# Kernel tuning notes

Measured on AMD Instinct MI355X. Metric: run time of the kernel, lower is better.

## Reference

```python
import jax, jax.numpy as jnp
import numpy as np

EPS = 1e-5


def _bn(x, g, b):
    # training-mode BatchNorm2d over (N, H, W), biased variance
    m = jnp.mean(x, axis=(0, 2, 3), keepdims=True)
    v = jnp.var(x, axis=(0, 2, 3), keepdims=True)
    return (x - m) * jax.lax.rsqrt(v + EPS) * g[None, :, None, None] + b[None, :, None, None]


def _conv1x1(x, w):
    # x: [B, Cin, H, W], w: [Cout, Cin]
    return jnp.einsum('bchw,oc->bohw', x, w)


def _prop_attention(x, wq, wkv, wo, bo, obj_dict, bg_dict, rand_inds):
    B, C, H, W = x.shape  # B == 1
    heads, crop = rand_inds.shape[0], rand_inds.shape[1]
    dh = C // heads
    HW = H * W
    num_obj = crop // 2
    # original does x.clone().detach() before attention
    xd = jax.lax.stop_gradient(x)
    xh = xd.reshape(heads, dh, HW)  # batch=1 folded away (matches t.view(-1, crop**2))
    # pos[h, i, j] = flat pixel index gathered for head h, group i, slot j
    pos = jnp.concatenate(
        [obj_dict[rand_inds[:, :num_obj]], bg_dict[rand_inds[:, num_obj:]]], axis=1
    )  # [heads, crop, crop]
    tokens = jax.vmap(lambda xv, pv: xv[:, pv])(xh, pos)  # [heads, dh, crop, crop]
    tokens = tokens.transpose(0, 2, 3, 1).reshape(heads * crop, crop, dh)
    q = tokens @ wq.T
    k, v = jnp.split(tokens @ wkv.T, 2, axis=-1)
    dots = jnp.einsum('bie,bje->bij', q, k) * (dh ** -0.5)
    attn = jax.nn.softmax(dots, axis=-1)
    out = jnp.einsum('bij,bje->bie', attn, v)  # [heads*crop, crop, dh]
    # faithful to torch out.view(heads*crop, -1, crop): a raw row-major reinterpret
    out_r = out.reshape(heads, crop, dh, crop)
    vals = out_r.transpose(0, 2, 1, 3).reshape(heads, dh, crop * crop)
    pos_flat = pos.reshape(heads, crop * crop)
    # pos is a bijection onto [0, HW) per head -> invert and gather
    ar = jnp.arange(HW, dtype=jnp.int32)
    inv = jax.vmap(lambda p: jnp.zeros((HW,), jnp.int32).at[p].set(ar))(pos_flat)
    img = jax.vmap(lambda vh, ih: vh[:, ih])(vals, inv)  # [heads, dh, HW]
    img = img.reshape(1, heads * dh, H, W)
    # to_out: Linear(dim, dim) applied channels-last
    return jnp.einsum('bchw,oc->bohw', img, wo) + bo[None, :, None, None]


def setup_inputs():
    H = W = 300
    HW = H * W
    heads, crop = 2, H
    num_obj = crop // 2
    ch, emb = 256, 64
    dh = emb // heads
    key = jax.random.key(0)
    ks = jax.random.split(key, 10)
    x = jax.random.normal(ks[0], (1, ch, H, W), jnp.float32)
    perm = jax.random.permutation(ks[1], HW)
    obj_dict = perm[: HW // 2]
    bg_dict = perm[HW // 2 :]
    ri = []
    for h in range(heads):
        po = jax.random.permutation(jax.random.fold_in(ks[2], h), HW // 2).reshape(num_obj, crop)
        pb = jax.random.permutation(jax.random.fold_in(ks[3], h), HW // 2).reshape(crop - num_obj, crop)
        ri.append(jnp.concatenate([po, pb], axis=0))
    rand_inds = jnp.stack(ri)  # [heads, crop, crop]
    w_conv1 = jax.random.normal(ks[4], (emb, ch), jnp.float32) / np.sqrt(ch)
    wq = jax.random.normal(ks[5], (dh, dh), jnp.float32) / np.sqrt(dh)
    wkv = jax.random.normal(ks[6], (2 * dh, dh), jnp.float32) / np.sqrt(dh)
    wo = jax.random.normal(ks[7], (emb, emb), jnp.float32) / np.sqrt(emb)
    bo = jnp.zeros((emb,), jnp.float32)
    w_conv2 = jax.random.normal(ks[8], (emb, 2 * emb), jnp.float32) / np.sqrt(2 * emb)
    return {
        'x': x,
        'w_conv1': w_conv1,
        'bn1_g': jnp.ones((emb,), jnp.float32),
        'bn1_b': jnp.zeros((emb,), jnp.float32),
        'wq': wq,
        'wkv': wkv,
        'wo': wo,
        'bo': bo,
        'w_conv2': w_conv2,
        'bn2_g': jnp.ones((emb,), jnp.float32),
        'bn2_b': jnp.zeros((emb,), jnp.float32),
        'obj_dict': obj_dict,
        'bg_dict': bg_dict,
        'rand_inds': rand_inds,
    }


def reference(x, w_conv1, bn1_g, bn1_b, wq, wkv, wo, bo, w_conv2, bn2_g, bn2_b, obj_dict, bg_dict, rand_inds):
    x1 = jax.nn.relu(_bn(_conv1x1(x, w_conv1), bn1_g, bn1_b))
    xa = jax.nn.relu(_prop_attention(x1, wq, wkv, wo, bo, obj_dict, bg_dict, rand_inds))
    xc = jnp.concatenate([xa, x1], axis=1)
    return jax.nn.relu(_bn(_conv1x1(xc, w_conv2), bn2_g, bn2_b))
```

## Files before the change

kernel.cpp:

```cpp
#include <hip/hip_runtime.h>
#include <hip/hip_bf16.h>

#define HW 90000
#define CROP 300
#define C2EXP 0.25503492f

typedef __attribute__((ext_vector_type(8))) short s8v;
typedef __attribute__((ext_vector_type(4))) float f4v;
#define MFMA16(a,b,c) __builtin_amdgcn_mfma_f32_16x16x32_bf16(a,b,c,0,0,0)

__device__ __forceinline__ unsigned short f2bf(float f) {
    unsigned int u = __float_as_uint(f);
    return (unsigned short)((u + 0x7fffu + ((u >> 16) & 1u)) >> 16);
}
__device__ __forceinline__ float bf2f(unsigned short s) {
    return __uint_as_float(((unsigned int)s) << 16);
}
__device__ __forceinline__ unsigned pk_trunc(float a, float b) {
    return __builtin_amdgcn_perm(__float_as_uint(b), __float_as_uint(a), 0x07060302u);
}
__device__ __forceinline__ unsigned pk_rne(float a, float b) {
    return (unsigned)f2bf(a) | ((unsigned)f2bf(b) << 16);
}

__global__ void prep_kernel(const float* __restrict__ w1, const float* __restrict__ wq,
                            const float* __restrict__ wkv, const float* __restrict__ wo,
                            const float* __restrict__ w2,
                            short* __restrict__ w1b, short* __restrict__ wkvb,
                            short* __restrict__ wob, short* __restrict__ w2b,
                            short* __restrict__ msb) {
    int idx = blockIdx.x * blockDim.x + threadIdx.x;
    int stride = gridDim.x * blockDim.x;
    for (int i = idx; i < 16384; i += stride) w1b[i] = (short)f2bf(w1[i]);
    for (int i = idx; i < 2048; i += stride)  wkvb[i] = (short)f2bf(wkv[i]);
    for (int i = idx; i < 4096; i += stride)  wob[i] = (short)f2bf(wo[i]);
    for (int i = idx; i < 8192; i += stride)  w2b[i] = (short)f2bf(w2[i]);
    for (int i = idx; i < 1024; i += stride) {
        int ep = i >> 5, e = i & 31;
        float s = 0.f;
        for (int a = 0; a < 32; ++a) s += wq[a * 32 + e] * wkv[a * 32 + ep];
        msb[i] = (short)f2bf(s * C2EXP);
    }
}

__global__ __launch_bounds__(256, 4) void conv1_mfma(const float* __restrict__ x,
        const short* __restrict__ w1b, short* __restrict__ y1b, float* __restrict__ stat) {
    __shared__ __align__(16) short lw[16384];
    __shared__ float red[2][4][64];
    const int wave = threadIdx.x >> 6, lane = threadIdx.x & 63;
    const int q = lane >> 4, n = lane & 15;
    for (int i = threadIdx.x; i < 2048; i += 256)
        ((uint4*)lw)[i] = ((const uint4*)w1b)[i];
    __syncthreads();

    const int s0 = blockIdx.x * 128 + wave * 32;
    int pbx = s0 + 2 * n;
    if (pbx > HW - 2) pbx = HW - 2;
    f4v acc[2][4];
#pragma unroll
    for (int mt = 0; mt < 2; ++mt)
#pragma unroll
        for (int nt = 0; nt < 4; ++nt) acc[mt][nt] = f4v{0.f, 0.f, 0.f, 0.f};

    float2 cur[8], nxt[8];
#pragma unroll
    for (int j = 0; j < 8; ++j)
        cur[j] = *(const float2*)(x + (size_t)(q * 8 + j) * HW + pbx);
#pragma unroll
    for (int kb = 0; kb < 8; ++kb) {
        if (kb < 7) {
#pragma unroll
            for (int j = 0; j < 8; ++j)
                nxt[j] = *(const float2*)(x + (size_t)((kb + 1) * 32 + q * 8 + j) * HW + pbx);
        }
        s8v A[2];
        {
            union { unsigned u[4]; s8v v; } a0, a1;
#pragma unroll
            for (int w = 0; w < 4; ++w) {
                a0.u[w] = pk_trunc(cur[2 * w].x, cur[2 * w + 1].x);
                a1.u[w] = pk_trunc(cur[2 * w].y, cur[2 * w + 1].y);
            }
            A[0] = a0.v; A[1] = a1.v;
        }
#pragma unroll
        for (int nt = 0; nt < 4; ++nt) {
            int c = (nt & 1) + 2 * n + 32 * (nt >> 1);
            s8v B = *(const s8v*)(lw + c * 256 + kb * 32 + q * 8);
            acc[0][nt] = MFMA16(A[0], B, acc[0][nt]);
            acc[1][nt] = MFMA16(A[1], B, acc[1][nt]);
        }
        if (kb < 7) {
#pragma unroll
            for (int j = 0; j < 8; ++j) cur[j] = nxt[j];
        }
    }

    float s1[4] = {0.f, 0.f, 0.f, 0.f}, s2[4] = {0.f, 0.f, 0.f, 0.f};
#pragma unroll
    for (int mt = 0; mt < 2; ++mt)
#pragma unroll
        for (int r = 0; r < 4; ++r) {
            int p = s0 + 2 * (q * 4 + r) + mt;
            if (p < HW) {
                float v0 = acc[mt][0][r], v1 = acc[mt][1][r];
                float v2 = acc[mt][2][r], v3 = acc[mt][3][r];
                *(unsigned*)(y1b + (size_t)p * 64 + 2 * n)      = pk_rne(v0, v1);
                *(unsigned*)(y1b + (size_t)p * 64 + 32 + 2 * n) = pk_rne(v2, v3);
                s1[0] += v0; s2[0] += v0 * v0;
                s1[1] += v1; s2[1] += v1 * v1;
                s1[2] += v2; s2[2] += v2 * v2;
                s1[3] += v3; s2[3] += v3 * v3;
            }
        }
#pragma unroll
    for (int m = 16; m < 64; m <<= 1)
#pragma unroll
        for (int nt = 0; nt < 4; ++nt) {
            s1[nt] += __shfl_xor(s1[nt], m, 64);
            s2[nt] += __shfl_xor(s2[nt], m, 64);
        }
    if (lane < 16)
#pragma unroll
        for (int nt = 0; nt < 4; ++nt) {
            int c = (nt & 1) + 2 * lane + 32 * (nt >> 1);
            red[0][wave][c] = s1[nt];
            red[1][wave][c] = s2[nt];
        }
    __syncthreads();
    if (threadIdx.x < 128) {
        int k = threadIdx.x >> 6, c = threadIdx.x & 63;
        atomicAdd(&stat[k * 64 + c],
                  red[k][0][c] + red[k][1][c] + red[k][2][c] + red[k][3][c]);
    }
}

__global__ void bn_fin_kernel(const float* __restrict__ stat,
        const float* __restrict__ g, const float* __restrict__ b, float* __restrict__ ab) {
    int c = threadIdx.x;
    float m = stat[c] * (1.f / HW);
    float v = stat[64 + c] * (1.f / HW) - m * m;
    float ac = g[c] * rsqrtf(v + 1e-5f);
    ab[c] = ac;
    ab[64 + c] = b[c] - m * ac;
}

__global__ __launch_bounds__(256) void bnrelu_kernel(const short* __restrict__ y1b,
        const float* __restrict__ ab1, short* __restrict__ x1b) {
    int t = blockIdx.x * 256 + threadIdx.x;
    if (t >= 720000) return;
    int cb = 8 * (t & 7);
    float4 a0 = *(const float4*)(ab1 + cb), a1 = *(const float4*)(ab1 + cb + 4);
    float4 b0 = *(const float4*)(ab1 + 64 + cb), b1 = *(const float4*)(ab1 + 64 + cb + 4);
    uint4 u = ((const uint4*)y1b)[t];
    float r0 = fmaxf(fmaf(a0.x, __uint_as_float(u.x << 16), b0.x), 0.f);
    float r1 = fmaxf(fmaf(a0.y, __uint_as_float(u.x & 0xffff0000u), b0.y), 0.f);
    float r2 = fmaxf(fmaf(a0.z, __uint_as_float(u.y << 16), b0.z), 0.f);
    float r3 = fmaxf(fmaf(a0.w, __uint_as_float(u.y & 0xffff0000u), b0.w), 0.f);
    float r4 = fmaxf(fmaf(a1.x, __uint_as_float(u.z << 16), b1.x), 0.f);
    float r5 = fmaxf(fmaf(a1.y, __uint_as_float(u.z & 0xffff0000u), b1.y), 0.f);
    float r6 = fmaxf(fmaf(a1.z, __uint_as_float(u.w << 16), b1.z), 0.f);
    float r7 = fmaxf(fmaf(a1.w, __uint_as_float(u.w & 0xffff0000u), b1.w), 0.f);
    uint4 o;
    o.x = pk_rne(r0, r1); o.y = pk_rne(r2, r3);
    o.z = pk_rne(r4, r5); o.w = pk_rne(r6, r7);
    ((uint4*)x1b)[t] = o;
}

__global__ __launch_bounds__(384, 4) void attn_mfma_kernel(const short* __restrict__ x1b,
        const short* __restrict__ msb, const short* __restrict__ wkvb,
        const int* __restrict__ obj, const int* __restrict__ bg,
        const int* __restrict__ rinds, short* __restrict__ imgb) {
    __shared__ __align__(16) short tok[304 * 40];
    __shared__ __align__(16) short vt[32 * 328];
    __shared__ __align__(16) short pbuf[6 * 16 * 40];
    __shared__ int possh[300];
    const int b = blockIdx.x;
    const int h = b / CROP, i = b - h * CROP;
    const int tid = threadIdx.x;
    const int wave = tid >> 6, lane = tid & 63, q = lane >> 4, n = lane & 15;

    if (tid < 300) {
        int ri = rinds[h * HW + i * CROP + tid];
        possh[tid] = (i < 150) ? obj[ri] : bg[ri];
    }
    for (int ii = tid; ii < 80; ii += 384)
        ((unsigned*)(tok + 300 * 40))[ii] = 0;
    for (int ii = tid; ii < 640; ii += 384) {
        int e = ii / 20, w = ii - 20 * e;
        ((unsigned*)vt)[e * 164 + 144 + w] = 0;
    }
    __syncthreads();

    for (int idx = tid; idx < 1200; idx += 384) {
        int j = idx >> 2, part = idx & 3;
        *(uint4*)(tok + j * 40 + part * 8) =
            *(const uint4*)(x1b + (size_t)possh[j] * 64 + h * 32 + part * 8);
    }
    __syncthreads();

    short* pw = pbuf + wave * 16 * 40;
    s8v aQ[4];
    {
        s8v bq0 = *(const s8v*)(msb + n * 32 + q * 8);
        s8v bq1 = *(const s8v*)(msb + (16 + n) * 32 + q * 8);
        s8v bv0 = *(const s8v*)(wkvb + (32 + n) * 32 + q * 8);
        s8v bv1 = *(const s8v*)(wkvb + (48 + n) * 32 + q * 8);
        f4v zz = {0.f, 0.f, 0.f, 0.f};
#pragma unroll
        for (int ti = 0; ti < 4; ++ti) {
            int t = wave + ti * 6;
            aQ[ti] = s8v{};
            if (t < 19) {
                s8v at = *(const s8v*)(tok + (16 * t + n) * 40 + q * 8);
                f4v qf0 = MFMA16(at, bq0, zz);
                f4v qf1 = MFMA16(at, bq1, zz);
                f4v vf0 = MFMA16(at, bv0, zz);
                f4v vf1 = MFMA16(at, bv1, zz);
#pragma unroll
                for (int r = 0; r < 4; ++r) {
                    int row = 16 * t + q * 4 + r;
                    int phys = ((row >> 5) << 5) + 2 * (row & 15) + ((row >> 4) & 1);
                    vt[n * 328 + phys]        = (short)f2bf(vf0[r]);
                    vt[(16 + n) * 328 + phys] = (short)f2bf(vf1[r]);
                    pw[(q * 4 + r) * 40 + n]      = (short)f2bf(qf0[r]);
                    pw[(q * 4 + r) * 40 + 16 + n] = (short)f2bf(qf1[r]);
                }
                asm volatile("s_waitcnt lgkmcnt(0)" ::: "memory");
                aQ[ti] = *(const s8v*)(pw + n * 40 + q * 8);
            }
        }
    }
    __syncthreads();

    f4v O[4][2];
    float lsum[4][4];
#pragma unroll
    for (int ti = 0; ti < 4; ++ti) {
        O[ti][0] = f4v{0.f, 0.f, 0.f, 0.f};
        O[ti][1] = f4v{0.f, 0.f, 0.f, 0.f};
#pragma unroll
        for (int r = 0; r < 4; ++r) lsum[ti][r] = 0.f;
    }
    unsigned* pwd = (unsigned*)pw;
    f4v zz = {0.f, 0.f, 0.f, 0.f};
    for (int kb = 0; kb < 10; ++kb) {
        s8v bK0 = *(const s8v*)(tok + (32 * kb + n) * 40 + q * 8);
        s8v bK1 = (kb < 9) ? *(const s8v*)(tok + (32 * kb + 16 + n) * 40 + q * 8) : s8v{};
        s8v bV0 = *(const s8v*)(vt + n * 328 + kb * 32 + q * 8);
        s8v bV1 = *(const s8v*)(vt + (16 + n) * 328 + kb * 32 + q * 8);
#pragma unroll
        for (int ti = 0; ti < 4; ++ti) {
            int t = wave + ti * 6;
            if (t >= 19) continue;
            f4v s0 = MFMA16(aQ[ti], bK0, zz);
            if (kb < 9) {
                f4v s1 = MFMA16(aQ[ti], bK1, zz);
#pragma unroll
                for (int r = 0; r < 4; ++r) {
                    float e0 = exp2f(s0[r]);
                    float e1 = exp2f(s1[r]);
                    unsigned pk = pk_trunc(e0, e1);
                    lsum[ti][r] += __uint_as_float(pk << 16) +
                                   __uint_as_float(pk & 0xffff0000u);
                    pwd[(q * 4 + r) * 20 + n] = pk;
                }
            } else {
#pragma unroll
                for (int r = 0; r < 4; ++r) {
                    float e0 = (n < 12) ? exp2f(s0[r]) : 0.f;
                    unsigned pk = pk_trunc(e0, 0.f);
                    lsum[ti][r] += __uint_as_float(pk << 16);
                    pwd[(q * 4 + r) * 20 + n] = pk;
                }
            }
            asm volatile("s_waitcnt lgkmcnt(0)" ::: "memory");
            s8v ap = *(const s8v*)(pw + n * 40 + q * 8);
            O[ti][0] = MFMA16(ap, bV0, O[ti][0]);
            O[ti][1] = MFMA16(ap, bV1, O[ti][1]);
        }
    }
    __syncthreads();

#pragma unroll
    for (int m = 1; m < 16; m <<= 1) {
#pragma unroll
        for (int ti = 0; ti < 4; ++ti)
#pragma unroll
            for (int r = 0; r < 4; ++r)
                lsum[ti][r] += __shfl_xor(lsum[ti][r], m, 64);
    }
    short* outb = tok;
#pragma unroll
    for (int ti = 0; ti < 4; ++ti) {
        int t = wave + ti * 6;
        if (t >= 19) continue;
#pragma unroll
        for (int r = 0; r < 4; ++r) {
            float rl = 1.f / lsum[ti][r];
            int row = 16 * t + q * 4 + r;
            outb[row * 32 + n]      = (short)f2bf(O[ti][0][r] * rl);
            outb[row * 32 + 16 + n] = (short)f2bf(O[ti][1][r] * rl);
        }
    }
    __syncthreads();

    for (int idx = tid; idx < 9600; idx += 384) {
        int jj = idx >> 5, dd = idx & 31;
        imgb[(size_t)possh[jj] * 64 + h * 32 + dd] = outb[dd * CROP + jj];
    }
}

__global__ __launch_bounds__(256, 2) void fuse2_mfma(const short* __restrict__ imgb,
        const short* __restrict__ x1b,
        const short* __restrict__ wob, const short* __restrict__ w2b,
        const float* __restrict__ bo, float* __restrict__ y2, float* __restrict__ stat) {
    __shared__ __align__(16) short xas[4][16 * 72];
    __shared__ float ytr[64 * 133];
    __shared__ float red[2][4][64];
    const int wave = threadIdx.x >> 6, lane = threadIdx.x & 63;
    const int q = lane >> 4, n = lane & 15;
    s8v Bo[2][4], B2[4][4];
#pragma unroll
    for (int kb = 0; kb < 2; ++kb)
#pragma unroll
        for (int nt = 0; nt < 4; ++nt)
            Bo[kb][nt] = *(const s8v*)(wob + (nt * 16 + n) * 64 + kb * 32 + q * 8);
#pragma unroll
    for (int kb = 0; kb < 4; ++kb)
#pragma unroll
        for (int nt = 0; nt < 4; ++nt)
            B2[kb][nt] = *(const s8v*)(w2b + (nt * 16 + n) * 128 + kb * 32 + q * 8);
    float bov[4];
#pragma unroll
    for (int nt = 0; nt < 4; ++nt) bov[nt] = bo[nt * 16 + n];

    float s1[4] = {0.f, 0.f, 0.f, 0.f}, s2[4] = {0.f, 0.f, 0.f, 0.f};
    short* xw = xas[wave];
#pragma unroll
    for (int ti = 0; ti < 2; ++ti) {
        int tile = blockIdx.x * 8 + wave * 2 + ti;
        if (tile >= 5625) continue;
        int s0 = tile * 16;
        f4v xacc[4];
#pragma unroll
        for (int nt = 0; nt < 4; ++nt) xacc[nt] = f4v{0.f, 0.f, 0.f, 0.f};
#pragma unroll
        for (int kb = 0; kb < 2; ++kb) {
            s8v A = *(const s8v*)(imgb + (size_t)(s0 + n) * 64 + kb * 32 + q * 8);
#pragma unroll
            for (int nt = 0; nt < 4; ++nt) xacc[nt] = MFMA16(A, Bo[kb][nt], xacc[nt]);
        }
#pragma unroll
        for (int nt = 0; nt < 4; ++nt)
#pragma unroll
            for (int r = 0; r < 4; ++r) {
                float v = fmaxf(xacc[nt][r] + bov[nt], 0.f);
                xw[(q * 4 + r) * 72 + nt * 16 + n] = (short)f2bf(v);
            }
        asm volatile("s_waitcnt lgkmcnt(0)" ::: "memory");
        f4v yacc[4];
#pragma unroll
        for (int nt = 0; nt < 4; ++nt) yacc[nt] = f4v{0.f, 0.f, 0.f, 0.f};
#pragma unroll
        for (int kb = 0; kb < 2; ++kb) {
            s8v Axa = *(const s8v*)(xw + n * 72 + kb * 32 + q * 8);
#pragma unroll
            for (int nt = 0; nt < 4; ++nt) yacc[nt] = MFMA16(Axa, B2[kb][nt], yacc[nt]);
        }
#pragma unroll
        for (int kb = 0; kb < 2; ++kb) {
            s8v A = *(const s8v*)(x1b + (size_t)(s0 + n) * 64 + kb * 32 + q * 8);
#pragma unroll
            for (int nt = 0; nt < 4; ++nt) yacc[nt] = MFMA16(A, B2[kb + 2][nt], yacc[nt]);
        }
        int pl = wave * 32 + ti * 16;
#pragma unroll
        for (int nt = 0; nt < 4; ++nt)
#pragma unroll
            for (int r = 0; r < 4; ++r) {
                float v = yacc[nt][r];
                s1[nt] += v; s2[nt] += v * v;
                ytr[(nt * 16 + n) * 133 + pl + q * 4 + r] = v;
            }
    }
#pragma unroll
    for (int m = 16; m < 64; m <<= 1)
#pragma unroll
        for (int nt = 0; nt < 4; ++nt) {
            s1[nt] += __shfl_xor(s1[nt], m, 64);
            s2[nt] += __shfl_xor(s2[nt], m, 64);
        }
    if (lane < 16)
#pragma unroll
        for (int nt = 0; nt < 4; ++nt) {
            red[0][wave][nt * 16 + lane] = s1[nt];
            red[1][wave][nt * 16 + lane] = s2[nt];
        }
    __syncthreads();
    int s0b = blockIdx.x * 128;
    for (int i = threadIdx.x; i < 8192; i += 256) {
        int c = i >> 7, p = i & 127;
        int s = s0b + p;
        if (s < HW) y2[(size_t)c * HW + s] = ytr[c * 133 + p];
    }
    if (threadIdx.x < 128) {
        int k = threadIdx.x >> 6, c = threadIdx.x & 63;
        atomicAdd(&stat[k * 64 + c],
                  red[k][0][c] + red[k][1][c] + red[k][2][c] + red[k][3][c]);
    }
}

__global__ __launch_bounds__(256) void bn_out_kernel(const float* __restrict__ y2,
        const float* __restrict__ ab2, float* __restrict__ out) {
    int c = blockIdx.y;
    int s4 = blockIdx.x * 256 + threadIdx.x;
    if (s4 >= 22500) return;
    float a = ab2[c], b = ab2[64 + c];
    float4 v = *(const float4*)(y2 + (size_t)c * HW + s4 * 4);
    v.x = fmaxf(fmaf(a, v.x, b), 0.f);
    v.y = fmaxf(fmaf(a, v.y, b), 0.f);
    v.z = fmaxf(fmaf(a, v.z, b), 0.f);
    v.w = fmaxf(fmaf(a, v.w, b), 0.f);
    *(float4*)(out + (size_t)c * HW + s4 * 4) = v;
}

extern "C" void kernel_launch(void* const* d_in, const int* in_sizes, int n_in,
                              void* d_out, int out_size, void* d_ws, size_t ws_size,
                              hipStream_t stream) {
    const float* x   = (const float*)d_in[0];
    const float* w1  = (const float*)d_in[1];
    const float* g1  = (const float*)d_in[2];
    const float* b1  = (const float*)d_in[3];
    const float* wq  = (const float*)d_in[4];
    const float* wkv = (const float*)d_in[5];
    const float* wo  = (const float*)d_in[6];
    const float* bo  = (const float*)d_in[7];
    const float* w2  = (const float*)d_in[8];
    const float* g2  = (const float*)d_in[9];
    const float* b2  = (const float*)d_in[10];
    const int* obj   = (const int*)d_in[11];
    const int* bg    = (const int*)d_in[12];
    const int* rinds = (const int*)d_in[13];

    float* WSF  = (float*)d_ws;
    short* W1B  = (short*)d_ws;
    short* WOB  = W1B + 16384;
    short* W2B  = WOB + 4096;
    short* WKVB = W2B + 8192;
    short* MSB  = WKVB + 2048;
    float* STAT = WSF + 16384;
    float* AB1  = STAT + 256;
    float* AB2  = AB1 + 128;
    short* Y1B  = (short*)(WSF + 16896);
    short* X1B  = Y1B + 5760000;
    short* IMGB = X1B + 5760000;
    float* Y2   = WSF + 16896 + 8640000;

    hipMemsetAsync(STAT, 0, 1024, stream);
    prep_kernel<<<16, 256, 0, stream>>>(w1, wq, wkv, wo, w2, W1B, WKVB, WOB, W2B, MSB);
    conv1_mfma<<<704, 256, 0, stream>>>(x, W1B, Y1B, STAT);
    bn_fin_kernel<<<1, 64, 0, stream>>>(STAT, g1, b1, AB1);
    bnrelu_kernel<<<2813, 256, 0, stream>>>(Y1B, AB1, X1B);
    attn_mfma_kernel<<<600, 384, 0, stream>>>(X1B, MSB, WKVB, obj, bg, rinds, IMGB);
    fuse2_mfma<<<704, 256, 0, stream>>>(IMGB, X1B, WOB, W2B, bo, Y2, STAT + 128);
    bn_fin_kernel<<<1, 64, 0, stream>>>(STAT + 128, g2, b2, AB2);
    bn_out_kernel<<<dim3(88, 64), 256, 0, stream>>>(Y2, AB2, (float*)d_out);
}
```

Before: 271.5 us.

## Widen conv1 tiles, use 8 waves in attention, store pre-BN conv2 output as bf16

Three separate changes. conv1 now handles 256 pixels per block, with float4 loads and four M-tiles per wave, so it launches half as many blocks. The attention kernel goes from 6 to 8 waves; each wave works through up to 3 query tiles and batches the score MFMAs, exp and PV steps across those tiles to reduce serialised LDS waits. The intermediate conv2 output is now written as packed bf16 rather than fp32, which halves its write and read traffic through bn_out but adds a bf16 rounding step before the second BatchNorm.

New measurement: 253.0 us. -6.8%, faster.

```diff
diff --git a/kernel.cpp b/kernel.cpp
--- a/kernel.cpp
+++ b/kernel.cpp
@@ -43,7 +43,7 @@
     }
 }
 
-__global__ __launch_bounds__(256, 4) void conv1_mfma(const float* __restrict__ x,
+__global__ __launch_bounds__(256, 2) void conv1_mfma(const float* __restrict__ x,
         const short* __restrict__ w1b, short* __restrict__ y1b, float* __restrict__ stat) {
     __shared__ __align__(16) short lw[16384];
     __shared__ float red[2][4][64];
@@ -53,43 +53,44 @@
         ((uint4*)lw)[i] = ((const uint4*)w1b)[i];
     __syncthreads();
 
-    const int s0 = blockIdx.x * 128 + wave * 32;
-    int pbx = s0 + 2 * n;
-    if (pbx > HW - 2) pbx = HW - 2;
-    f4v acc[2][4];
-#pragma unroll
-    for (int mt = 0; mt < 2; ++mt)
+    const int s0 = blockIdx.x * 256 + wave * 64;
+    int pbx = s0 + 4 * n;
+    if (pbx > HW - 4) pbx = HW - 4;
+    f4v acc[4][4];
+#pragma unroll
+    for (int mt = 0; mt < 4; ++mt)
 #pragma unroll
         for (int nt = 0; nt < 4; ++nt) acc[mt][nt] = f4v{0.f, 0.f, 0.f, 0.f};
 
-    float2 cur[8], nxt[8];
+    float4 cur[8], nxt[8];
 #pragma unroll
     for (int j = 0; j < 8; ++j)
-        cur[j] = *(const float2*)(x + (size_t)(q * 8 + j) * HW + pbx);
+        cur[j] = *(const float4*)(x + (size_t)(q * 8 + j) * HW + pbx);
 #pragma unroll
     for (int kb = 0; kb < 8; ++kb) {
         if (kb < 7) {
 #pragma unroll
             for (int j = 0; j < 8; ++j)
-                nxt[j] = *(const float2*)(x + (size_t)((kb + 1) * 32 + q * 8 + j) * HW + pbx);
-        }
-        s8v A[2];
-        {
-            union { unsigned u[4]; s8v v; } a0, a1;
-#pragma unroll
-            for (int w = 0; w < 4; ++w) {
-                a0.u[w] = pk_trunc(cur[2 * w].x, cur[2 * w + 1].x);
-                a1.u[w] = pk_trunc(cur[2 * w].y, cur[2 * w + 1].y);
-            }
-            A[0] = a0.v; A[1] = a1.v;
-        }
-#pragma unroll
-        for (int nt = 0; nt < 4; ++nt) {
-            int c = (nt & 1) + 2 * n + 32 * (nt >> 1);
-            s8v B = *(const s8v*)(lw + c * 256 + kb * 32 + q * 8);
-            acc[0][nt] = MFMA16(A[0], B, acc[0][nt]);
-            acc[1][nt] = MFMA16(A[1], B, acc[1][nt]);
-        }
+                nxt[j] = *(const float4*)(x + (size_t)((kb + 1) * 32 + q * 8 + j) * HW + pbx);
+        }
+        s8v A[4];
+#pragma unroll
+        for (int mt = 0; mt < 4; ++mt) {
+            union { unsigned u[4]; s8v v; } am;
+#pragma unroll
+            for (int w = 0; w < 4; ++w)
+                am.u[w] = pk_trunc(((const float*)&cur[2 * w])[mt],
+                                   ((const float*)&cur[2 * w + 1])[mt]);
+            A[mt] = am.v;
+        }
+#pragma unroll
+        for (int mt = 0; mt < 4; ++mt)
+#pragma unroll
+            for (int nt = 0; nt < 4; ++nt) {
+                int c = (nt & 1) + 2 * n + 32 * (nt >> 1);
+                s8v B = *(const s8v*)(lw + c * 256 + kb * 32 + q * 8);
+                acc[mt][nt] = MFMA16(A[mt], B, acc[mt][nt]);
+            }
         if (kb < 7) {
 #pragma unroll
             for (int j = 0; j < 8; ++j) cur[j] = nxt[j];
@@ -98,10 +99,10 @@
 
     float s1[4] = {0.f, 0.f, 0.f, 0.f}, s2[4] = {0.f, 0.f, 0.f, 0.f};
 #pragma unroll
-    for (int mt = 0; mt < 2; ++mt)
+    for (int mt = 0; mt < 4; ++mt)
 #pragma unroll
         for (int r = 0; r < 4; ++r) {
-            int p = s0 + 2 * (q * 4 + r) + mt;
+            int p = s0 + 4 * (q * 4 + r) + mt;
             if (p < HW) {
                 float v0 = acc[mt][0][r], v1 = acc[mt][1][r];
                 float v2 = acc[mt][2][r], v3 = acc[mt][3][r];
@@ -167,40 +168,41 @@
     ((uint4*)x1b)[t] = o;
 }
 
-__global__ __launch_bounds__(384, 4) void attn_mfma_kernel(const short* __restrict__ x1b,
+__global__ __launch_bounds__(512, 4) void attn_mfma_kernel(const short* __restrict__ x1b,
         const short* __restrict__ msb, const short* __restrict__ wkvb,
         const int* __restrict__ obj, const int* __restrict__ bg,
         const int* __restrict__ rinds, short* __restrict__ imgb) {
     __shared__ __align__(16) short tok[304 * 40];
     __shared__ __align__(16) short vt[32 * 328];
-    __shared__ __align__(16) short pbuf[6 * 16 * 40];
+    __shared__ __align__(16) short pbuf[8 * 3 * 640];
     __shared__ int possh[300];
     const int b = blockIdx.x;
     const int h = b / CROP, i = b - h * CROP;
     const int tid = threadIdx.x;
     const int wave = tid >> 6, lane = tid & 63, q = lane >> 4, n = lane & 15;
+    const int nti = (wave < 3) ? 3 : 2;
 
     if (tid < 300) {
         int ri = rinds[h * HW + i * CROP + tid];
         possh[tid] = (i < 150) ? obj[ri] : bg[ri];
     }
-    for (int ii = tid; ii < 80; ii += 384)
+    for (int ii = tid; ii < 80; ii += 512)
         ((unsigned*)(tok + 300 * 40))[ii] = 0;
-    for (int ii = tid; ii < 640; ii += 384) {
+    for (int ii = tid; ii < 640; ii += 512) {
         int e = ii / 20, w = ii - 20 * e;
         ((unsigned*)vt)[e * 164 + 144 + w] = 0;
     }
     __syncthreads();
 
-    for (int idx = tid; idx < 1200; idx += 384) {
+    for (int idx = tid; idx < 1200; idx += 512) {
         int j = idx >> 2, part = idx & 3;
         *(uint4*)(tok + j * 40 + part * 8) =
             *(const uint4*)(x1b + (size_t)possh[j] * 64 + h * 32 + part * 8);
     }
     __syncthreads();
 
-    short* pw = pbuf + wave * 16 * 40;
-    s8v aQ[4];
+    short* pw0 = pbuf + wave * 3 * 640;
+    s8v aQ[3];
     {
         s8v bq0 = *(const s8v*)(msb + n * 32 + q * 8);
         s8v bq1 = *(const s8v*)(msb + (16 + n) * 32 + q * 8);
@@ -208,10 +210,10 @@
         s8v bv1 = *(const s8v*)(wkvb + (48 + n) * 32 + q * 8);
         f4v zz = {0.f, 0.f, 0.f, 0.f};
 #pragma unroll
-        for (int ti = 0; ti < 4; ++ti) {
-            int t = wave + ti * 6;
+        for (int ti = 0; ti < 3; ++ti) {
             aQ[ti] = s8v{};
-            if (t < 19) {
+            if (ti < nti) {
+                int t = wave + ti * 8;
                 s8v at = *(const s8v*)(tok + (16 * t + n) * 40 + q * 8);
                 f4v qf0 = MFMA16(at, bq0, zz);
                 f4v qf1 = MFMA16(at, bq1, zz);
@@ -223,78 +225,86 @@
                     int phys = ((row >> 5) << 5) + 2 * (row & 15) + ((row >> 4) & 1);
                     vt[n * 328 + phys]        = (short)f2bf(vf0[r]);
                     vt[(16 + n) * 328 + phys] = (short)f2bf(vf1[r]);
-                    pw[(q * 4 + r) * 40 + n]      = (short)f2bf(qf0[r]);
-                    pw[(q * 4 + r) * 40 + 16 + n] = (short)f2bf(qf1[r]);
+                    pw0[(q * 4 + r) * 40 + n]      = (short)f2bf(qf0[r]);
+                    pw0[(q * 4 + r) * 40 + 16 + n] = (short)f2bf(qf1[r]);
                 }
                 asm volatile("s_waitcnt lgkmcnt(0)" ::: "memory");
-                aQ[ti] = *(const s8v*)(pw + n * 40 + q * 8);
-            }
-        }
-    }
-    __syncthreads();
-
-    f4v O[4][2];
-    float lsum[4][4];
-#pragma unroll
-    for (int ti = 0; ti < 4; ++ti) {
+                aQ[ti] = *(const s8v*)(pw0 + n * 40 + q * 8);
+            }
+        }
+    }
+    __syncthreads();
+
+    f4v O[3][2];
+    float lsum[3][4];
+#pragma unroll
+    for (int ti = 0; ti < 3; ++ti) {
         O[ti][0] = f4v{0.f, 0.f, 0.f, 0.f};
         O[ti][1] = f4v{0.f, 0.f, 0.f, 0.f};
 #pragma unroll
         for (int r = 0; r < 4; ++r) lsum[ti][r] = 0.f;
     }
-    unsigned* pwd = (unsigned*)pw;
     f4v zz = {0.f, 0.f, 0.f, 0.f};
     for (int kb = 0; kb < 10; ++kb) {
         s8v bK0 = *(const s8v*)(tok + (32 * kb + n) * 40 + q * 8);
         s8v bK1 = (kb < 9) ? *(const s8v*)(tok + (32 * kb + 16 + n) * 40 + q * 8) : s8v{};
         s8v bV0 = *(const s8v*)(vt + n * 328 + kb * 32 + q * 8);
         s8v bV1 = *(const s8v*)(vt + (16 + n) * 328 + kb * 32 + q * 8);
-#pragma unroll
-        for (int ti = 0; ti < 4; ++ti) {
-            int t = wave + ti * 6;
-            if (t >= 19) continue;
-            f4v s0 = MFMA16(aQ[ti], bK0, zz);
-            if (kb < 9) {
-                f4v s1 = MFMA16(aQ[ti], bK1, zz);
-#pragma unroll
-                for (int r = 0; r < 4; ++r) {
-                    float e0 = exp2f(s0[r]);
-                    float e1 = exp2f(s1[r]);
-                    unsigned pk = pk_trunc(e0, e1);
-                    lsum[ti][r] += __uint_as_float(pk << 16) +
-                                   __uint_as_float(pk & 0xffff0000u);
-                    pwd[(q * 4 + r) * 20 + n] = pk;
+        f4v sv[3][2];
+#pragma unroll
+        for (int ti = 0; ti < 3; ++ti)
+            if (ti < nti) {
+                sv[ti][0] = MFMA16(aQ[ti], bK0, zz);
+                sv[ti][1] = MFMA16(aQ[ti], bK1, zz);
+            }
+#pragma unroll
+        for (int ti = 0; ti < 3; ++ti)
+            if (ti < nti) {
+                unsigned* pwd = (unsigned*)(pbuf + (wave * 3 + ti) * 640);
+                if (kb < 9) {
+#pragma unroll
+                    for (int r = 0; r < 4; ++r) {
+                        float e0 = exp2f(sv[ti][0][r]);
+                        float e1 = exp2f(sv[ti][1][r]);
+                        unsigned pk = pk_trunc(e0, e1);
+                        lsum[ti][r] += __uint_as_float(pk << 16) +
+                                       __uint_as_float(pk & 0xffff0000u);
+                        pwd[(q * 4 + r) * 20 + n] = pk;
+                    }
+                } else {
+#pragma unroll
+                    for (int r = 0; r < 4; ++r) {
+                        float e0 = (n < 12) ? exp2f(sv[ti][0][r]) : 0.f;
+                        unsigned pk = pk_trunc(e0, 0.f);
+                        lsum[ti][r] += __uint_as_float(pk << 16);
+                        pwd[(q * 4 + r) * 20 + n] = pk;
+                    }
                 }
-            } else {
-#pragma unroll
-                for (int r = 0; r < 4; ++r) {
-                    float e0 = (n < 12) ? exp2f(s0[r]) : 0.f;
-                    unsigned pk = pk_trunc(e0, 0.f);
-                    lsum[ti][r] += __uint_as_float(pk << 16);
-                    pwd[(q * 4 + r) * 20 + n] = pk;
-                }
-            }
-            asm volatile("s_waitcnt lgkmcnt(0)" ::: "memory");
-            s8v ap = *(const s8v*)(pw + n * 40 + q * 8);
-            O[ti][0] = MFMA16(ap, bV0, O[ti][0]);
-            O[ti][1] = MFMA16(ap, bV1, O[ti][1]);
-        }
+            }
+        asm volatile("s_waitcnt lgkmcnt(0)" ::: "memory");
+#pragma unroll
+        for (int ti = 0; ti < 3; ++ti)
+            if (ti < nti) {
+                s8v ap = *(const s8v*)(pbuf + (wave * 3 + ti) * 640 + n * 40 + q * 8);
+                O[ti][0] = MFMA16(ap, bV0, O[ti][0]);
+                O[ti][1] = MFMA16(ap, bV1, O[ti][1]);
+            }
     }
     __syncthreads();
 
 #pragma unroll
     for (int m = 1; m < 16; m <<= 1) {
 #pragma unroll
-        for (int ti = 0; ti < 4; ++ti)
+        for (int ti = 0; ti < 3; ++ti)
 #pragma unroll
             for (int r = 0; r < 4; ++r)
                 lsum[ti][r] += __shfl_xor(lsum[ti][r], m, 64);
     }
     short* outb = tok;
 #pragma unroll
-    for (int ti = 0; ti < 4; ++ti) {
-        int t = wave + ti * 6;
-        if (t >= 19) continue;
+    for (int ti = 0; ti < 3; ++ti) {
+        if (ti >= nti) continue;
+        int t = wave + ti * 8;
 #pragma unroll
         for (int r = 0; r < 4; ++r) {
             float rl = 1.f / lsum[ti][r];
@@ -305,18 +315,18 @@
     }
     __syncthreads();
 
-    for (int idx = tid; idx < 9600; idx += 384) {
+    for (int idx = tid; idx < 9600; idx += 512) {
         int jj = idx >> 5, dd = idx & 31;
         imgb[(size_t)possh[jj] * 64 + h * 32 + dd] = outb[dd * CROP + jj];
     }
 }
 
-__global__ __launch_bounds__(256, 2) void fuse2_mfma(const short* __restrict__ imgb,
+__global__ __launch_bounds__(256, 3) void fuse2_mfma(const short* __restrict__ imgb,
         const short* __restrict__ x1b,
         const short* __restrict__ wob, const short* __restrict__ w2b,
-        const float* __restrict__ bo, float* __restrict__ y2, float* __restrict__ stat) {
+        const float* __restrict__ bo, short* __restrict__ y2b, float* __restrict__ stat) {
     __shared__ __align__(16) short xas[4][16 * 72];
-    __shared__ float ytr[64 * 133];
+    __shared__ unsigned ytrp[64 * 68];
     __shared__ float red[2][4][64];
     const int wave = threadIdx.x >> 6, lane = threadIdx.x & 63;
     const int q = lane >> 4, n = lane & 15;
@@ -374,15 +384,17 @@
 #pragma unroll
             for (int nt = 0; nt < 4; ++nt) yacc[nt] = MFMA16(A, B2[kb + 2][nt], yacc[nt]);
         }
-        int pl = wave * 32 + ti * 16;
-#pragma unroll
-        for (int nt = 0; nt < 4; ++nt)
+        int pl2 = wave * 16 + ti * 8;
+#pragma unroll
+        for (int nt = 0; nt < 4; ++nt) {
 #pragma unroll
             for (int r = 0; r < 4; ++r) {
                 float v = yacc[nt][r];
                 s1[nt] += v; s2[nt] += v * v;
-                ytr[(nt * 16 + n) * 133 + pl + q * 4 + r] = v;
-            }
+            }
+            ytrp[(nt * 16 + n) * 68 + pl2 + q * 2 + 0] = pk_rne(yacc[nt][0], yacc[nt][1]);
+            ytrp[(nt * 16 + n) * 68 + pl2 + q * 2 + 1] = pk_rne(yacc[nt][2], yacc[nt][3]);
+        }
     }
 #pragma unroll
     for (int m = 16; m < 64; m <<= 1)
@@ -399,10 +411,11 @@
         }
     __syncthreads();
     int s0b = blockIdx.x * 128;
-    for (int i = threadIdx.x; i < 8192; i += 256) {
-        int c = i >> 7, p = i & 127;
-        int s = s0b + p;
-        if (s < HW) y2[(size_t)c * HW + s] = ytr[c * 133 + p];
+    int maxp2 = (HW - s0b) >> 1;
+    for (int i = threadIdx.x; i < 4096; i += 256) {
+        int c = i >> 6, p2 = i & 63;
+        if (p2 < maxp2)
+            ((unsigned*)y2b)[c * (HW / 2) + (s0b >> 1) + p2] = ytrp[c * 68 + p2];
     }
     if (threadIdx.x < 128) {
         int k = threadIdx.x >> 6, c = threadIdx.x & 63;
@@ -411,18 +424,19 @@
     }
 }
 
-__global__ __launch_bounds__(256) void bn_out_kernel(const float* __restrict__ y2,
+__global__ __launch_bounds__(256) void bn_out_kernel(const short* __restrict__ y2b,
         const float* __restrict__ ab2, float* __restrict__ out) {
     int c = blockIdx.y;
-    int s4 = blockIdx.x * 256 + threadIdx.x;
-    if (s4 >= 22500) return;
+    int i = blockIdx.x * 256 + threadIdx.x;
+    if (i >= 22500) return;
     float a = ab2[c], b = ab2[64 + c];
-    float4 v = *(const float4*)(y2 + (size_t)c * HW + s4 * 4);
-    v.x = fmaxf(fmaf(a, v.x, b), 0.f);
-    v.y = fmaxf(fmaf(a, v.y, b), 0.f);
-    v.z = fmaxf(fmaf(a, v.z, b), 0.f);
-    v.w = fmaxf(fmaf(a, v.w, b), 0.f);
-    *(float4*)(out + (size_t)c * HW + s4 * 4) = v;
+    uint2 u = *(const uint2*)((const unsigned*)y2b + c * (HW / 2) + 2 * i);
+    float4 v;
+    v.x = fmaxf(fmaf(a, __uint_as_float(u.x << 16), b), 0.f);
+    v.y = fmaxf(fmaf(a, __uint_as_float(u.x & 0xffff0000u), b), 0.f);
+    v.z = fmaxf(fmaf(a, __uint_as_float(u.y << 16), b), 0.f);
+    v.w = fmaxf(fmaf(a, __uint_as_float(u.y & 0xffff0000u), b), 0.f);
+    *(float4*)(out + (size_t)c * HW + 4 * i) = v;
 }
 
 extern "C" void kernel_launch(void* const* d_in, const int* in_sizes, int n_in,
@@ -455,15 +469,15 @@
     short* Y1B  = (short*)(WSF + 16896);
     short* X1B  = Y1B + 5760000;
     short* IMGB = X1B + 5760000;
-    float* Y2   = WSF + 16896 + 8640000;
+    short* Y2B  = IMGB + 5760000;
 
     hipMemsetAsync(STAT, 0, 1024, stream);
     prep_kernel<<<16, 256, 0, stream>>>(w1, wq, wkv, wo, w2, W1B, WKVB, WOB, W2B, MSB);
-    conv1_mfma<<<704, 256, 0, stream>>>(x, W1B, Y1B, STAT);
+    conv1_mfma<<<352, 256, 0, stream>>>(x, W1B, Y1B, STAT);
     bn_fin_kernel<<<1, 64, 0, stream>>>(STAT, g1, b1, AB1);
     bnrelu_kernel<<<2813, 256, 0, stream>>>(Y1B, AB1, X1B);
-    attn_mfma_kernel<<<600, 384, 0, stream>>>(X1B, MSB, WKVB, obj, bg, rinds, IMGB);
-    fuse2_mfma<<<704, 256, 0, stream>>>(IMGB, X1B, WOB, W2B, bo, Y2, STAT + 128);
+    attn_mfma_kernel<<<600, 512, 0, stream>>>(X1B, MSB, WKVB, obj, bg, rinds, IMGB);
+    fuse2_mfma<<<704, 256, 0, stream>>>(IMGB, X1B, WOB, W2B, bo, Y2B, STAT + 128);
     bn_fin_kernel<<<1, 64, 0, stream>>>(STAT + 128, g2, b2, AB2);
-    bn_out_kernel<<<dim3(88, 64), 256, 0, stream>>>(Y2, AB2, (float*)d_out);
-}
+    bn_out_kernel<<<dim3(88, 64), 256, 0, stream>>>(Y2B, AB2, (float*)d_out);
+}
```
